# Kernel optimization log

Measured on AMD Instinct MI355X. Metric: run time of the kernel, lower is better.

The kernel has to match this reference:

```python
import jax, jax.numpy as jnp
import numpy as np

MAX_BITS = 64
HIDDEN = 256
EPS = 1e-5
TEMPERATURE = 1.0  # buffer default


def _layernorm(x, gamma, beta):
    mu = jnp.mean(x, axis=-1, keepdims=True)
    var = jnp.var(x, axis=-1, keepdims=True)
    return (x - mu) * jax.lax.rsqrt(var + EPS) * gamma + beta


def setup_inputs() -> dict:
    key = jax.random.key(0)
    ks = jax.random.split(key, 8)
    B = 32768
    # binary-ish inputs in [0,1)
    a_bits = (jax.random.uniform(ks[0], (B, MAX_BITS)) < 0.5).astype(jnp.float32)
    shift_bits = (jax.random.uniform(ks[1], (B, MAX_BITS)) < 0.5).astype(jnp.float32)
    # decoder: Linear(64,256) -> LN -> ReLU -> Linear(256,256) -> LN -> ReLU -> Linear(256,64)
    def lin(k, out_d, in_d):
        bound = 1.0 / np.sqrt(in_d)
        kw, kb = jax.random.split(k)
        W = jax.random.uniform(kw, (out_d, in_d), minval=-bound, maxval=bound)
        b = jax.random.uniform(kb, (out_d,), minval=-bound, maxval=bound)
        return W, b
    W1, b1 = lin(ks[2], HIDDEN, MAX_BITS)
    W2, b2 = lin(ks[3], HIDDEN, HIDDEN)
    W3, b3 = lin(ks[4], MAX_BITS, HIDDEN)
    g1 = jnp.ones((HIDDEN,)); be1 = jnp.zeros((HIDDEN,))
    g2 = jnp.ones((HIDDEN,)); be2 = jnp.zeros((HIDDEN,))
    return {
        "a_bits": a_bits, "shift_bits": shift_bits,
        "W1": W1, "b1": b1, "g1": g1, "be1": be1,
        "W2": W2, "b2": b2, "g2": g2, "be2": be2,
        "W3": W3, "b3": b3,
    }


def reference(a_bits, shift_bits, W1, b1, g1, be1, W2, b2, g2, be2, W3, b3):
    bits = a_bits.shape[1]
    # 2-layer MLP decoder
    h = jax.nn.relu(_layernorm(shift_bits @ W1.T + b1, g1, be1))
    h = jax.nn.relu(_layernorm(h @ W2.T + b2, g2, be2))
    shift_logits = (h @ W3.T + b3)[:, :bits]
    # training path: softmax over shift positions
    shift_probs = jax.nn.softmax(shift_logits / TEMPERATURE, axis=-1)
    # Toeplitz shift-sum: out[b,i] = sum_{s<=i} probs[b,s] * a_bits[b,i-s]
    i = jnp.arange(bits)[:, None]
    s = jnp.arange(bits)[None, :]
    idx = i - s                       # [bits, bits]
    mask = (idx >= 0)
    gath = a_bits[:, jnp.where(mask, idx, 0)] * mask.astype(a_bits.dtype)  # [B, bits, bits]
    return jnp.einsum('bis,bs->bi', gath, shift_probs)
```

## Files before the change

kernel.cpp:

```cpp
#include <hip/hip_runtime.h>
#include <hip/hip_fp16.h>


typedef short s8v __attribute__((ext_vector_type(8)));
typedef float f4v __attribute__((ext_vector_type(4)));

#define HPAD 264
#define PPAD 68

#define OFF_W1F 0
#define OFF_W2F 16384
#define OFF_W3F 81920
#define OFF_B1  98304
#define OFF_G1  98560
#define OFF_BE1 98816
#define OFF_B2  99072
#define OFF_G2  99328
#define OFF_BE2 99584
#define OFF_B3  99840

__device__ __forceinline__ float b2f(unsigned short u) {
    union { unsigned int i; float f; } v; v.i = ((unsigned int)u) << 16; return v.f;
}
__device__ __forceinline__ unsigned short f2b(float f) {
    union { float f; unsigned int i; } v; v.f = f;
    return (unsigned short)((v.i + 0x7fffu + ((v.i >> 16) & 1u)) >> 16);
}
__device__ __forceinline__ unsigned int cvtpk(float a, float b) {
    unsigned int r;
    asm("v_cvt_pk_bf16_f32 %0, %1, %2" : "=v"(r) : "v"(a), "v"(b));
    return r;
}
__device__ __forceinline__ int h2i(__half2 h) { union { __half2 h; int i; } u; u.h = h; return u.i; }
__device__ __forceinline__ __half2 i2h(int i) { union { __half2 h; int i; } u; u.i = i; return u.h; }

__device__ __forceinline__ bool probe_bf16(const void* a_bits) {
    unsigned int wv = ((const unsigned int*)a_bits)[threadIdx.x & 63];
    return __ballot((wv & 0xffffu) == 0x3f80u) != 0ULL;
}

__global__ __launch_bounds__(256) void convert_kernel(
    const void* __restrict__ a_probe,
    const void* __restrict__ W1, const void* __restrict__ W2, const void* __restrict__ W3,
    const void* __restrict__ b1, const void* __restrict__ g1, const void* __restrict__ be1,
    const void* __restrict__ b2, const void* __restrict__ g2, const void* __restrict__ be2,
    const void* __restrict__ b3,
    unsigned short* __restrict__ ws)
{
    const bool isbf = probe_bf16(a_probe);
    const int t = blockIdx.x * 256 + threadIdx.x;

    if (t < 12288) {
        const void* W; int K, idx, dstbase;
        if (t < 2048)       { idx = t;         W = W1; K = 64;  dstbase = OFF_W1F + idx * 8; }
        else if (t < 10240) { idx = t - 2048;  W = W2; K = 256; dstbase = OFF_W2F + idx * 8; }
        else                { idx = t - 10240; W = W3; K = 256; dstbase = OFF_W3F + idx * 8; }
        int nt, kc, lane;
        if (t < 2048) { nt = idx >> 7; kc = (idx >> 6) & 1; lane = idx & 63; }
        else          { nt = idx >> 9; kc = (idx >> 6) & 7; lane = idx & 63; }
        const int row = nt * 16 + (lane & 15);
        const int col = kc * 32 + (lane >> 4) * 8;
        const int src = row * K + col;
        s8v o;
        if (isbf) {
            o = *(const s8v*)((const unsigned short*)W + src);
        } else {
            const float* f = (const float*)W + src;
#pragma unroll
            for (int j = 0; j < 8; ++j) o[j] = (short)f2b(f[j]);
        }
        *(s8v*)(ws + dstbase) = o;
    } else if (t < 12488) {
        const int v = t - 12288;
        const void* srcp; int base, off;
        if (v < 32)       { srcp = b1;  base = OFF_B1;  off = v * 8; }
        else if (v < 64)  { srcp = g1;  base = OFF_G1;  off = (v - 32) * 8; }
        else if (v < 96)  { srcp = be1; base = OFF_BE1; off = (v - 64) * 8; }
        else if (v < 128) { srcp = b2;  base = OFF_B2;  off = (v - 96) * 8; }
        else if (v < 160) { srcp = g2;  base = OFF_G2;  off = (v - 128) * 8; }
        else if (v < 192) { srcp = be2; base = OFF_BE2; off = (v - 160) * 8; }
        else              { srcp = b3;  base = OFF_B3;  off = (v - 192) * 8; }
#pragma unroll
        for (int j = 0; j < 8; ++j)
            ws[base + off + j] = isbf ? ((const unsigned short*)srcp)[off + j]
                                      : f2b(((const float*)srcp)[off + j]);
    }
}

template<bool BF16>
__device__ __forceinline__ float loadS(const void* p, int idx) {
    if constexpr (BF16) return b2f(((const unsigned short*)p)[idx]);
    else return ((const float*)p)[idx];
}
template<bool BF16>
__device__ __forceinline__ s8v loadA8(const void* p, int idx) {
    if constexpr (BF16) {
        return *(const s8v*)((const unsigned short*)p + idx);
    } else {
        const float* f = (const float*)p + idx;
        f4v a = *(const f4v*)f;
        f4v b = *(const f4v*)(f + 4);
        union { s8v s; unsigned int u[4]; } r;
        r.u[0] = cvtpk(a[0], a[1]);
        r.u[1] = cvtpk(a[2], a[3]);
        r.u[2] = cvtpk(b[0], b[1]);
        r.u[3] = cvtpk(b[2], b[3]);
        return r.s;
    }
}
template<bool BF16>
__device__ __forceinline__ void storeO(void* p, int idx, float v) {
    if constexpr (BF16) ((unsigned short*)p)[idx] = f2b(v);
    else ((float*)p)[idx] = v;
}

template<bool BF16>
__device__ __forceinline__ void pipeline(
    const void* a_bits, const void* shifts, const unsigned short* ws, void* out,
    short* Hs, float* Ps, float* SS)
{
    const int tid = threadIdx.x;
    const int h = tid >> 6;
    const int l = tid & 63;
    const int q = l >> 4;
    const int c = l & 15;
    const int ntb = h << 2;
    const int grow0 = (int)blockIdx.x << 4;
    const int row = q * 4;

    f4v acc1[4];
#pragma unroll
    for (int i = 0; i < 4; ++i) acc1[i] = (f4v){0.f, 0.f, 0.f, 0.f};

    const s8v xa0 = loadA8<BF16>(shifts, (grow0 + c) * 64 + q * 8);
    const s8v xa1 = loadA8<BF16>(shifts, (grow0 + c) * 64 + 32 + q * 8);
#pragma unroll
    for (int i = 0; i < 4; ++i) {
        const int nt = ntb + i;
        s8v wb0 = *(const s8v*)(ws + OFF_W1F + ((nt * 2 + 0) * 64 + l) * 8);
        s8v wb1 = *(const s8v*)(ws + OFF_W1F + ((nt * 2 + 1) * 64 + l) * 8);
        acc1[i] = __builtin_amdgcn_mfma_f32_16x16x32_bf16(xa0, wb0, acc1[i], 0, 0, 0);
        acc1[i] = __builtin_amdgcn_mfma_f32_16x16x32_bf16(xa1, wb1, acc1[i], 0, 0, 0);
    }
    {
        float s[4] = {0, 0, 0, 0}, ss[4] = {0, 0, 0, 0};
#pragma unroll
        for (int i = 0; i < 4; ++i) {
            float bias = b2f(ws[OFF_B1 + (ntb + i) * 16 + c]);
#pragma unroll
            for (int r = 0; r < 4; ++r) {
                float v = acc1[i][r] + bias;
                acc1[i][r] = v;
                s[r] += v; ss[r] += v * v;
            }
        }
#pragma unroll
        for (int m = 1; m <= 8; m <<= 1)
#pragma unroll
            for (int r = 0; r < 4; ++r) {
                s[r]  += __shfl_xor(s[r],  m, 64);
                ss[r] += __shfl_xor(ss[r], m, 64);
            }
        if (c == 0)
#pragma unroll
            for (int r = 0; r < 4; ++r) {
                SS[(h * 16 + row + r) * 2 + 0] = s[r];
                SS[(h * 16 + row + r) * 2 + 1] = ss[r];
            }
        __syncthreads();
#pragma unroll
        for (int r = 0; r < 4; ++r) {
            float st = 0.f, sq = 0.f;
#pragma unroll
            for (int wv = 0; wv < 4; ++wv) {
                st += SS[(wv * 16 + row + r) * 2 + 0];
                sq += SS[(wv * 16 + row + r) * 2 + 1];
            }
            float mean = st * (1.0f / 256.0f);
            float var  = fmaxf(sq * (1.0f / 256.0f) - mean * mean, 0.0f);
            s[r] = mean; ss[r] = rsqrtf(var + 1e-5f);
        }
#pragma unroll
        for (int i = 0; i < 4; ++i) {
            const int nt = ntb + i;
            float gg = b2f(ws[OFF_G1 + nt * 16 + c]);
            float bb = b2f(ws[OFF_BE1 + nt * 16 + c]);
            float y[4];
#pragma unroll
            for (int r = 0; r < 4; ++r)
                y[r] = fmaxf((acc1[i][r] - s[r]) * ss[r] * gg + bb, 0.0f);
            unsigned int u01 = cvtpk(y[0], y[1]);
            unsigned int u23 = cvtpk(y[2], y[3]);
            Hs[(row + 0) * HPAD + nt * 16 + c] = (short)(u01 & 0xffffu);
            Hs[(row + 1) * HPAD + nt * 16 + c] = (short)(u01 >> 16);
            Hs[(row + 2) * HPAD + nt * 16 + c] = (short)(u23 & 0xffffu);
            Hs[(row + 3) * HPAD + nt * 16 + c] = (short)(u23 >> 16);
        }
    }
    __syncthreads();

    f4v acc2[4];
#pragma unroll
    for (int i = 0; i < 4; ++i) acc2[i] = (f4v){0.f, 0.f, 0.f, 0.f};
#pragma unroll
    for (int ks = 0; ks < 8; ++ks) {
        s8v af = *(const s8v*)&Hs[c * HPAD + ks * 32 + q * 8];
#pragma unroll
        for (int i = 0; i < 4; ++i) {
            const int nt = ntb + i;
            s8v bf_ = *(const s8v*)(ws + OFF_W2F + ((nt * 8 + ks) * 64 + l) * 8);
            acc2[i] = __builtin_amdgcn_mfma_f32_16x16x32_bf16(af, bf_, acc2[i], 0, 0, 0);
        }
    }
    {
        float s[4] = {0, 0, 0, 0}, ss[4] = {0, 0, 0, 0};
#pragma unroll
        for (int i = 0; i < 4; ++i) {
            float bias = b2f(ws[OFF_B2 + (ntb + i) * 16 + c]);
#pragma unroll
            for (int r = 0; r < 4; ++r) {
                float v = acc2[i][r] + bias;
                acc2[i][r] = v;
                s[r] += v; ss[r] += v * v;
            }
        }
#pragma unroll
        for (int m = 1; m <= 8; m <<= 1)
#pragma unroll
            for (int r = 0; r < 4; ++r) {
                s[r]  += __shfl_xor(s[r],  m, 64);
                ss[r] += __shfl_xor(ss[r], m, 64);
            }
        if (c == 0)
#pragma unroll
            for (int r = 0; r < 4; ++r) {
                SS[(h * 16 + row + r) * 2 + 0] = s[r];
                SS[(h * 16 + row + r) * 2 + 1] = ss[r];
            }
        __syncthreads();
#pragma unroll
        for (int r = 0; r < 4; ++r) {
            float st = 0.f, sq = 0.f;
#pragma unroll
            for (int wv = 0; wv < 4; ++wv) {
                st += SS[(wv * 16 + row + r) * 2 + 0];
                sq += SS[(wv * 16 + row + r) * 2 + 1];
            }
            float mean = st * (1.0f / 256.0f);
            float var  = fmaxf(sq * (1.0f / 256.0f) - mean * mean, 0.0f);
            s[r] = mean; ss[r] = rsqrtf(var + 1e-5f);
        }
#pragma unroll
        for (int i = 0; i < 4; ++i) {
            const int nt = ntb + i;
            float gg = b2f(ws[OFF_G2 + nt * 16 + c]);
            float bb = b2f(ws[OFF_BE2 + nt * 16 + c]);
            float y[4];
#pragma unroll
            for (int r = 0; r < 4; ++r)
                y[r] = fmaxf((acc2[i][r] - s[r]) * ss[r] * gg + bb, 0.0f);
            unsigned int u01 = cvtpk(y[0], y[1]);
            unsigned int u23 = cvtpk(y[2], y[3]);
            Hs[(row + 0) * HPAD + nt * 16 + c] = (short)(u01 & 0xffffu);
            Hs[(row + 1) * HPAD + nt * 16 + c] = (short)(u01 >> 16);
            Hs[(row + 2) * HPAD + nt * 16 + c] = (short)(u23 & 0xffffu);
            Hs[(row + 3) * HPAD + nt * 16 + c] = (short)(u23 >> 16);
        }
    }
    __syncthreads();

    f4v acc3 = (f4v){0.f, 0.f, 0.f, 0.f};
#pragma unroll
    for (int ks = 0; ks < 8; ++ks) {
        s8v af = *(const s8v*)&Hs[c * HPAD + ks * 32 + q * 8];
        s8v bf_ = *(const s8v*)(ws + OFF_W3F + ((h * 8 + ks) * 64 + l) * 8);
        acc3 = __builtin_amdgcn_mfma_f32_16x16x32_bf16(af, bf_, acc3, 0, 0, 0);
    }
    {
        const float bias = b2f(ws[OFF_B3 + h * 16 + c]);
        float sum[4];
#pragma unroll
        for (int r = 0; r < 4; ++r) {
            float e = __expf(acc3[r] + bias);
            acc3[r] = e;
            sum[r] = e;
        }
#pragma unroll
        for (int m = 1; m <= 8; m <<= 1)
#pragma unroll
            for (int r = 0; r < 4; ++r)
                sum[r] += __shfl_xor(sum[r], m, 64);
        if (c == 0)
#pragma unroll
            for (int r = 0; r < 4; ++r)
                SS[(h * 16 + row + r) * 2 + 0] = sum[r];
        __syncthreads();
#pragma unroll
        for (int r = 0; r < 4; ++r) {
            float S = SS[(0 * 16 + row + r) * 2 + 0] + SS[(1 * 16 + row + r) * 2 + 0]
                    + SS[(2 * 16 + row + r) * 2 + 0] + SS[(3 * 16 + row + r) * 2 + 0];
            float inv = __builtin_amdgcn_rcpf(S);
            Ps[(row + r) * PPAD + h * 16 + c] = acc3[r] * inv;
        }
    }
    __syncthreads();

#pragma unroll
    for (int jj = 0; jj < 2; ++jj) {
        const int j = h * 2 + jj;
        const int m0 = j, m1 = j + 8;
        __half2 pph = __floats2half2_rn(Ps[m0 * PPAD + l], Ps[m1 * PPAD + l]);
        const int ppi = h2i(pph);
        __half2 aah = __floats2half2_rn(loadS<BF16>(a_bits, (grow0 + m0) * 64 + l),
                                        loadS<BF16>(a_bits, (grow0 + m1) * 64 + l));
        int rr = h2i(aah);
        __half2 acc = __float2half2_rn(0.0f);
#pragma unroll
        for (int s = 0; s < 64; ++s) {
            const int spi = __builtin_amdgcn_readlane(ppi, s);
            acc = __hfma2(i2h(spi), i2h(rr), acc);
            if (s < 63)
                rr = __builtin_amdgcn_update_dpp(0, rr, 0x138, 0xF, 0xF, true);
        }
        storeO<BF16>(out, (grow0 + m0) * 64 + l, __low2float(acc));
        storeO<BF16>(out, (grow0 + m1) * 64 + l, __high2float(acc));
    }
}

__global__ __launch_bounds__(256, 8) void shiftdec_kernel(
    const void* __restrict__ a_bits, const void* __restrict__ shifts,
    const unsigned short* __restrict__ ws, void* __restrict__ out)
{
    __shared__ __align__(16) char smem[16 * HPAD * 2];
    __shared__ __align__(16) float SSb[4 * 16 * 2];
    short* Hs = (short*)smem;
    float* Ps = (float*)smem;

    if (probe_bf16(a_bits))
        pipeline<true>(a_bits, shifts, ws, out, Hs, Ps, SSb);
    else
        pipeline<false>(a_bits, shifts, ws, out, Hs, Ps, SSb);
}

extern "C" void kernel_launch(void* const* d_in, const int* in_sizes, int n_in,
                              void* d_out, int out_size, void* d_ws, size_t ws_size,
                              hipStream_t stream) {
    const int B = in_sizes[0] / 64;
    const int grid = B / 16;

    hipLaunchKernelGGL(convert_kernel, dim3(49), dim3(256), 0, stream,
                       d_in[0], d_in[2], d_in[6], d_in[10],
                       d_in[3], d_in[4], d_in[5], d_in[7], d_in[8], d_in[9], d_in[11],
                       (unsigned short*)d_ws);
    hipLaunchKernelGGL(shiftdec_kernel, dim3(grid), dim3(256), 0, stream,
                       d_in[0], d_in[1], (const unsigned short*)d_ws, d_out);
}
```

Before: 115.7 us.

## Prefetch bias/LN params, a_bits and W2/W3 fragments into registers early

Moves global loads of the bias, gamma and beta values, the a_bits values and the first W2 / all W3 weight fragments to earlier points in the kernel, so their latency overlaps with MFMA and layernorm work instead of stalling later stages. This raises register pressure, so launch bounds are relaxed from 8 to 4 minimum blocks per SM. The trade-off is lower occupancy in exchange for more latency hiding within each wave.

```diff
diff --git a/kernel.cpp b/kernel.cpp
--- a/kernel.cpp
+++ b/kernel.cpp
@@ -128,6 +128,26 @@
     const int grow0 = (int)blockIdx.x << 4;
     const int row = q * 4;
 
+    float b1v[4], g1v[4], be1v[4], b2v[4], g2v[4], be2v[4];
+#pragma unroll
+    for (int i = 0; i < 4; ++i) {
+        const int o = (ntb + i) * 16 + c;
+        b1v[i]  = b2f(ws[OFF_B1  + o]);
+        g1v[i]  = b2f(ws[OFF_G1  + o]);
+        be1v[i] = b2f(ws[OFF_BE1 + o]);
+        b2v[i]  = b2f(ws[OFF_B2  + o]);
+        g2v[i]  = b2f(ws[OFF_G2  + o]);
+        be2v[i] = b2f(ws[OFF_BE2 + o]);
+    }
+    const float b3s = b2f(ws[OFF_B3 + h * 16 + c]);
+    float aj0[2], aj1[2];
+#pragma unroll
+    for (int jj = 0; jj < 2; ++jj) {
+        const int j = h * 2 + jj;
+        aj0[jj] = loadS<BF16>(a_bits, (grow0 + j) * 64 + l);
+        aj1[jj] = loadS<BF16>(a_bits, (grow0 + j + 8) * 64 + l);
+    }
+
     f4v acc1[4];
 #pragma unroll
     for (int i = 0; i < 4; ++i) acc1[i] = (f4v){0.f, 0.f, 0.f, 0.f};
@@ -142,14 +162,19 @@
         acc1[i] = __builtin_amdgcn_mfma_f32_16x16x32_bf16(xa0, wb0, acc1[i], 0, 0, 0);
         acc1[i] = __builtin_amdgcn_mfma_f32_16x16x32_bf16(xa1, wb1, acc1[i], 0, 0, 0);
     }
+
+    s8v w2pf[4];
+#pragma unroll
+    for (int i = 0; i < 4; ++i)
+        w2pf[i] = *(const s8v*)(ws + OFF_W2F + (((ntb + i) * 8 + 0) * 64 + l) * 8);
+
     {
         float s[4] = {0, 0, 0, 0}, ss[4] = {0, 0, 0, 0};
 #pragma unroll
         for (int i = 0; i < 4; ++i) {
-            float bias = b2f(ws[OFF_B1 + (ntb + i) * 16 + c]);
-#pragma unroll
-            for (int r = 0; r < 4; ++r) {
-                float v = acc1[i][r] + bias;
+#pragma unroll
+            for (int r = 0; r < 4; ++r) {
+                float v = acc1[i][r] + b1v[i];
                 acc1[i][r] = v;
                 s[r] += v; ss[r] += v * v;
             }
@@ -183,12 +208,10 @@
 #pragma unroll
         for (int i = 0; i < 4; ++i) {
             const int nt = ntb + i;
-            float gg = b2f(ws[OFF_G1 + nt * 16 + c]);
-            float bb = b2f(ws[OFF_BE1 + nt * 16 + c]);
             float y[4];
 #pragma unroll
             for (int r = 0; r < 4; ++r)
-                y[r] = fmaxf((acc1[i][r] - s[r]) * ss[r] * gg + bb, 0.0f);
+                y[r] = fmaxf((acc1[i][r] - s[r]) * ss[r] * g1v[i] + be1v[i], 0.0f);
             unsigned int u01 = cvtpk(y[0], y[1]);
             unsigned int u23 = cvtpk(y[2], y[3]);
             Hs[(row + 0) * HPAD + nt * 16 + c] = (short)(u01 & 0xffffu);
@@ -207,19 +230,24 @@
         s8v af = *(const s8v*)&Hs[c * HPAD + ks * 32 + q * 8];
 #pragma unroll
         for (int i = 0; i < 4; ++i) {
-            const int nt = ntb + i;
-            s8v bf_ = *(const s8v*)(ws + OFF_W2F + ((nt * 8 + ks) * 64 + l) * 8);
+            s8v bf_ = (ks == 0) ? w2pf[i]
+                    : *(const s8v*)(ws + OFF_W2F + (((ntb + i) * 8 + ks) * 64 + l) * 8);
             acc2[i] = __builtin_amdgcn_mfma_f32_16x16x32_bf16(af, bf_, acc2[i], 0, 0, 0);
         }
     }
+
+    s8v w3pf[8];
+#pragma unroll
+    for (int ks = 0; ks < 8; ++ks)
+        w3pf[ks] = *(const s8v*)(ws + OFF_W3F + ((h * 8 + ks) * 64 + l) * 8);
+
     {
         float s[4] = {0, 0, 0, 0}, ss[4] = {0, 0, 0, 0};
 #pragma unroll
         for (int i = 0; i < 4; ++i) {
-            float bias = b2f(ws[OFF_B2 + (ntb + i) * 16 + c]);
-#pragma unroll
-            for (int r = 0; r < 4; ++r) {
-                float v = acc2[i][r] + bias;
+#pragma unroll
+            for (int r = 0; r < 4; ++r) {
+                float v = acc2[i][r] + b2v[i];
                 acc2[i][r] = v;
                 s[r] += v; ss[r] += v * v;
             }
@@ -253,12 +281,10 @@
 #pragma unroll
         for (int i = 0; i < 4; ++i) {
             const int nt = ntb + i;
-            float gg = b2f(ws[OFF_G2 + nt * 16 + c]);
-            float bb = b2f(ws[OFF_BE2 + nt * 16 + c]);
             float y[4];
 #pragma unroll
             for (int r = 0; r < 4; ++r)
-                y[r] = fmaxf((acc2[i][r] - s[r]) * ss[r] * gg + bb, 0.0f);
+                y[r] = fmaxf((acc2[i][r] - s[r]) * ss[r] * g2v[i] + be2v[i], 0.0f);
             unsigned int u01 = cvtpk(y[0], y[1]);
             unsigned int u23 = cvtpk(y[2], y[3]);
             Hs[(row + 0) * HPAD + nt * 16 + c] = (short)(u01 & 0xffffu);
@@ -273,15 +299,13 @@
 #pragma unroll
     for (int ks = 0; ks < 8; ++ks) {
         s8v af = *(const s8v*)&Hs[c * HPAD + ks * 32 + q * 8];
-        s8v bf_ = *(const s8v*)(ws + OFF_W3F + ((h * 8 + ks) * 64 + l) * 8);
-        acc3 = __builtin_amdgcn_mfma_f32_16x16x32_bf16(af, bf_, acc3, 0, 0, 0);
+        acc3 = __builtin_amdgcn_mfma_f32_16x16x32_bf16(af, w3pf[ks], acc3, 0, 0, 0);
     }
     {
-        const float bias = b2f(ws[OFF_B3 + h * 16 + c]);
         float sum[4];
 #pragma unroll
         for (int r = 0; r < 4; ++r) {
-            float e = __expf(acc3[r] + bias);
+            float e = __expf(acc3[r] + b3s);
             acc3[r] = e;
             sum[r] = e;
         }
@@ -311,8 +335,7 @@
         const int m0 = j, m1 = j + 8;
         __half2 pph = __floats2half2_rn(Ps[m0 * PPAD + l], Ps[m1 * PPAD + l]);
         const int ppi = h2i(pph);
-        __half2 aah = __floats2half2_rn(loadS<BF16>(a_bits, (grow0 + m0) * 64 + l),
-                                        loadS<BF16>(a_bits, (grow0 + m1) * 64 + l));
+        __half2 aah = __floats2half2_rn(aj0[jj], aj1[jj]);
         int rr = h2i(aah);
         __half2 acc = __float2half2_rn(0.0f);
 #pragma unroll
@@ -327,7 +350,7 @@
     }
 }
 
-__global__ __launch_bounds__(256, 8) void shiftdec_kernel(
+__global__ __launch_bounds__(256, 4) void shiftdec_kernel(
     const void* __restrict__ a_bits, const void* __restrict__ shifts,
     const unsigned short* __restrict__ ws, void* __restrict__ out)
 {
```

Result: no change. 117.3 us (+1.4%).
